# Kernel optimization log

Measured on AMD Instinct MI355X. Metric: run time of the kernel, lower is better.

Reference implementation:

```python
import jax, jax.numpy as jnp
import numpy as np

B, S, F = 4, 512, 512
H, D = 8, 64          # num_heads, hidden_dim per head
R = 64                # number of relative-position buckets
OUT = 512


def setup_inputs() -> dict:
    key = jax.random.key(0)
    ks = jax.random.split(key, 12)
    sF = 1.0 / np.sqrt(F)
    sHD = 1.0 / np.sqrt(H * D)
    inp = {
        "key": jax.random.normal(ks[0], (B, S, F), jnp.float32),
        "value": jax.random.normal(ks[1], (B, S, F), jnp.float32),
        "query": jax.random.normal(ks[2], (B, S, F), jnp.float32),
        # padding mask: last 64 key positions masked out per batch element
        "mask": jnp.zeros((B, S), bool).at[:, S - 64:].set(True),
        "adj": jax.random.randint(ks[3], (B, S, S), 0, R, jnp.int64),
        "Wq": jax.random.normal(ks[4], (F, H * D), jnp.float32) * sF,
        "bq": jnp.zeros((H * D,), jnp.float32),
        "Wk": jax.random.normal(ks[5], (F, H * D), jnp.float32) * sF,
        "bk": jnp.zeros((H * D,), jnp.float32),
        "Wv": jax.random.normal(ks[6], (F, H * D), jnp.float32) * sF,
        "bv": jnp.zeros((H * D,), jnp.float32),
        "Wo": jax.random.normal(ks[7], (H * D, OUT), jnp.float32) * sHD,
        "bo": jnp.zeros((OUT,), jnp.float32),
        "emb_k": jax.random.normal(ks[8], (R, D), jnp.float32) * 0.02,
        "emb_v": jax.random.normal(ks[9], (R, D), jnp.float32) * 0.02,
    }
    return inp


def reference(key, value, query, mask, adj,
              Wq, bq, Wk, bk, Wv, bv, Wo, bo, emb_k, emb_v):
    b, s, _ = value.shape
    scale = 1.0 / np.sqrt(D)
    # projections -> [b, heads, seq, d]
    q = (query @ Wq + bq).reshape(b, s, H, D).transpose(0, 2, 1, 3)
    k = (key @ Wk + bk).reshape(b, s, H, D).transpose(0, 2, 1, 3)
    v = (value @ Wv + bv).reshape(b, s, H, D).transpose(0, 2, 1, 3)
    # content scores [b, h, q, k]
    scores = jnp.einsum('bhqd,bhkd->bhqk', q, k) * scale
    # relative-position key bias: emb_k[adj] is [b, q, k, d]
    a_k = emb_k[adj]
    scores = scores + jnp.einsum('bhqd,bqkd->bhqk', q, a_k) * scale
    # key-padding mask (True -> -inf), broadcast over heads and query rows
    scores = jnp.where(mask[:, None, None, :], jnp.asarray(-jnp.inf, scores.dtype), scores)
    attn = jax.nn.softmax(scores, axis=-1)  # dropout p=0 -> identity
    # context + relative-position value contribution
    ctx = jnp.einsum('bhqk,bhkd->bhqd', attn, v)
    a_v = emb_v[adj]  # [b, q, k, d]
    ctx = ctx + jnp.einsum('bhqk,bqkd->bhqd', attn, a_v)
    ctx = ctx.transpose(0, 2, 1, 3).reshape(b, s, H * D)
    out = ctx @ Wo + bo
    return out, attn
```

## Files before the change

### kernel.cpp

```cpp
#include <hip/hip_runtime.h>
#include <hip/hip_bf16.h>
#include <math.h>

#define BB 4
#define SS 512
#define HH 8
#define DD 64
#define RR 64
#define OO 512

typedef _Float16 f16;
typedef __attribute__((ext_vector_type(8))) _Float16 f16x8;
typedef __attribute__((ext_vector_type(4))) _Float16 f16x4;
typedef __attribute__((ext_vector_type(4))) float f32x4;

#define WS_QH    0u
#define WS_KH    (2u<<20)
#define WS_VTH   (4u<<20)
#define WS_CTXH  (6u<<20)
#define WS_ADJ8  (8u<<20)
#define WS_WT    (12u<<20)
#define WS_EVT   (14u<<20)

__device__ __forceinline__ int swz128(int row, int b)  { return row*128  + (b ^ ((row&7)<<4)); }
__device__ __forceinline__ int swz1024(int row, int b) { return row*1024 + (b ^ ((row&7)<<4)); }

__device__ __forceinline__ void pack8(const float4& x, const float4& y, f16x8& o) {
    o[0]=(f16)x.x; o[1]=(f16)x.y; o[2]=(f16)x.z; o[3]=(f16)x.w;
    o[4]=(f16)y.x; o[5]=(f16)y.y; o[6]=(f16)y.z; o[7]=(f16)y.w;
}

__global__ __launch_bounds__(256) void k_pack(const int* __restrict__ adj,
                                              const void* __restrict__ mask,
                                              unsigned char* __restrict__ adj8)
{
    const int tid = threadIdx.x;
    __shared__ int s_odd, s_big;
    if (tid == 0) { s_odd = 0; s_big = 0; }
    __syncthreads();
    int odd = 0, big = 0;
    const unsigned int* mu = (const unsigned int*)mask;
    for (int i = tid; i < 512; i += 256) {
        odd |= (adj[2*i + 1] != 0);
        big |= (mu[i] > 1u);
    }
    if (odd) atomicOr(&s_odd, 1);
    if (big) atomicOr(&s_big, 1);
    __syncthreads();
    const int f64 = s_odd ? 0 : 1;
    const int fbyte = s_big;

    const int t = blockIdx.x * 256 + tid;
    const int e0 = t * 4;
    const int b = e0 >> 18, k0 = e0 & 511;
    int a[4];
    if (f64) {
        const int4 A = ((const int4*)adj)[2*t];
        const int4 Bv = ((const int4*)adj)[2*t + 1];
        a[0] = A.x; a[1] = A.z; a[2] = Bv.x; a[3] = Bv.z;
    } else {
        const int4 A = ((const int4*)adj)[t];
        a[0] = A.x; a[1] = A.y; a[2] = A.z; a[3] = A.w;
    }
    unsigned int mbits;
    if (fbyte) {
        const unsigned int mw = *(const unsigned int*)((const unsigned char*)mask + b*512 + k0);
        mbits = ((mw & 255u) ? 1u : 0) | (((mw >> 8) & 255u) ? 2u : 0)
              | (((mw >> 16) & 255u) ? 4u : 0) | (((mw >> 24) & 255u) ? 8u : 0);
    } else {
        const int4 mv = ((const int4*)mask)[(b*512 + k0) >> 2];
        mbits = (mv.x ? 1u : 0) | (mv.y ? 2u : 0) | (mv.z ? 4u : 0) | (mv.w ? 8u : 0);
    }
    unsigned int w = 0;
#pragma unroll
    for (int j = 0; j < 4; ++j)
        w |= ((unsigned)(a[j] & 63) | (((mbits >> j) & 1u) << 7)) << (8*j);
    ((unsigned int*)adj8)[t] = w;
}

__global__ __launch_bounds__(256) void k_prep(
    const float* __restrict__ Wq, const float* __restrict__ Wk,
    const float* __restrict__ Wv, const float* __restrict__ Wo,
    const float* __restrict__ emb_v, f16* __restrict__ WT, f16* __restrict__ evt)
{
    const int z = blockIdx.z;
    __shared__ float tile[64][65];
    const int tid = threadIdx.x;
    const int r = tid >> 2, c4 = (tid & 3) * 16;
    if (z < 4) {
        const float* W = (z==0)?Wq:(z==1)?Wk:(z==2)?Wv:Wo;
        f16* T = WT + (size_t)z * 262144;
        const int k0 = blockIdx.y * 64, n0 = blockIdx.x * 64;
#pragma unroll
        for (int u = 0; u < 4; ++u) {
            const float4 w4 = *(const float4*)&W[(size_t)(k0 + r)*512 + n0 + c4 + u*4];
            tile[r][c4+u*4+0] = w4.x; tile[r][c4+u*4+1] = w4.y;
            tile[r][c4+u*4+2] = w4.z; tile[r][c4+u*4+3] = w4.w;
        }
        __syncthreads();
        f16x8 v0, v1;
#pragma unroll
        for (int j = 0; j < 8; ++j) { v0[j] = (f16)tile[c4+j][r]; v1[j] = (f16)tile[c4+8+j][r]; }
        f16* dst = &T[(size_t)(n0 + r)*512 + k0 + c4];
        *(f16x8*)dst = v0; *(f16x8*)(dst + 8) = v1;
    } else {
        if (blockIdx.x | blockIdx.y) return;
#pragma unroll
        for (int u = 0; u < 4; ++u) {
            const float4 w4 = *(const float4*)&emb_v[(size_t)r*64 + c4 + u*4];
            tile[r][c4+u*4+0] = w4.x; tile[r][c4+u*4+1] = w4.y;
            tile[r][c4+u*4+2] = w4.z; tile[r][c4+u*4+3] = w4.w;
        }
        __syncthreads();
        f16x8 v0, v1;
#pragma unroll
        for (int j = 0; j < 8; ++j) { v0[j] = (f16)tile[c4+j][r]; v1[j] = (f16)tile[c4+8+j][r]; }
        f16* dst = &evt[(size_t)r*64 + c4];
        *(f16x8*)dst = v0; *(f16x8*)(dst + 8) = v1;
    }
}

__global__ __launch_bounds__(256) void k_proj(
    const float* __restrict__ query, const float* __restrict__ key, const float* __restrict__ value,
    const f16* __restrict__ WT,
    const float* __restrict__ bq, const float* __restrict__ bk, const float* __restrict__ bv,
    f16* __restrict__ qh, f16* __restrict__ kh, f16* __restrict__ vth)
{
    const int z = blockIdx.z;
    const float* A    = (z == 0) ? query : (z == 1) ? key : value;
    const f16*   Bt   = WT + (size_t)z * 262144;
    const float* bias = (z == 0) ? bq : (z == 1) ? bk : bv;

    const int n0 = blockIdx.x * 64;
    const int m0 = blockIdx.y * 64;
    __shared__ char Ab[2][8192];
    __shared__ char Bb[2][8192];
    const int tid = threadIdx.x;
    const int wid = tid >> 6, l = tid & 63;
    const int wr = wid >> 1, wc = wid & 1;
    const int lr = l & 15, lg = l >> 4;
    const int sr = tid >> 2, sc = (tid & 3) * 16;

    const float* Ap = &A[(size_t)(m0 + sr)*512 + sc];
    const f16*   Bp = &Bt[(size_t)(n0 + sr)*512 + sc];

    f32x4 acc[2][2];
#pragma unroll
    for (int mi = 0; mi < 2; ++mi)
#pragma unroll
        for (int ni = 0; ni < 2; ++ni) acc[mi][ni] = (f32x4){0.f,0.f,0.f,0.f};

    float4 a4[4]; f16x8 b0, b1;
#pragma unroll
    for (int u = 0; u < 4; ++u) a4[u] = *(const float4*)(Ap + u*4);
    b0 = *(const f16x8*)Bp; b1 = *(const f16x8*)(Bp + 8);
    {
        f16x8 p0, p1;
        pack8(a4[0], a4[1], p0); pack8(a4[2], a4[3], p1);
        *(f16x8*)(Ab[0] + swz128(sr, sc*2))    = p0;
        *(f16x8*)(Ab[0] + swz128(sr, sc*2+16)) = p1;
        *(f16x8*)(Bb[0] + swz128(sr, sc*2))    = b0;
        *(f16x8*)(Bb[0] + swz128(sr, sc*2+16)) = b1;
    }
#pragma unroll
    for (int t = 0; t < 8; ++t) {
        __syncthreads();
        if (t < 7) {
#pragma unroll
            for (int u = 0; u < 4; ++u) a4[u] = *(const float4*)(Ap + (t+1)*64 + u*4);
            b0 = *(const f16x8*)(Bp + (t+1)*64);
            b1 = *(const f16x8*)(Bp + (t+1)*64 + 8);
        }
        const char* Ac = Ab[t & 1];
        const char* Bc = Bb[t & 1];
        f16x8 fa[2][2], fb[2][2];
#pragma unroll
        for (int mi = 0; mi < 2; ++mi) {
            const int row = wr*32 + mi*16 + lr;
#pragma unroll
            for (int ks = 0; ks < 2; ++ks)
                fa[mi][ks] = *(const f16x8*)(Ac + swz128(row, ks*64 + lg*16));
        }
#pragma unroll
        for (int ni = 0; ni < 2; ++ni) {
            const int row = wc*32 + ni*16 + lr;
#pragma unroll
            for (int ks = 0; ks < 2; ++ks)
                fb[ni][ks] = *(const f16x8*)(Bc + swz128(row, ks*64 + lg*16));
        }
#pragma unroll
        for (int ks = 0; ks < 2; ++ks)
#pragma unroll
            for (int mi = 0; mi < 2; ++mi)
#pragma unroll
                for (int ni = 0; ni < 2; ++ni)
                    acc[mi][ni] = __builtin_amdgcn_mfma_f32_16x16x32_f16(
                        fa[mi][ks], fb[ni][ks], acc[mi][ni], 0, 0, 0);
        if (t < 7) {
            f16x8 p0, p1;
            pack8(a4[0], a4[1], p0); pack8(a4[2], a4[3], p1);
            char* An = Ab[(t+1) & 1];
            char* Bn = Bb[(t+1) & 1];
            *(f16x8*)(An + swz128(sr, sc*2))    = p0;
            *(f16x8*)(An + swz128(sr, sc*2+16)) = p1;
            *(f16x8*)(Bn + swz128(sr, sc*2))    = b0;
            *(f16x8*)(Bn + swz128(sr, sc*2+16)) = b1;
        }
    }

#pragma unroll
    for (int ni = 0; ni < 2; ++ni) {
        const int n = n0 + wc*32 + ni*16 + lr;
        const float bv_ = bias[n];
        const int h = n >> 6, d = n & 63;
#pragma unroll
        for (int mi = 0; mi < 2; ++mi)
#pragma unroll
            for (int e = 0; e < 4; ++e) {
                const int m = m0 + wr*32 + mi*16 + lg*4 + e;
                const int b = m >> 9, s = m & 511;
                const f16 v = (f16)(acc[mi][ni][e] + bv_);
                if (z == 2)       vth[((size_t)(b*HH + h)*DD + d)*SS + s] = v;
                else if (z == 1)  kh [((size_t)(b*HH + h)*SS + s)*DD + d] = v;
                else              qh [((size_t)(b*HH + h)*SS + s)*DD + d] = v;
            }
    }
}

__global__ __launch_bounds__(256, 4) void k_attn(
    const f16* __restrict__ qh, const f16* __restrict__ kh, const f16* __restrict__ vth,
    const unsigned char* __restrict__ adj8, const float* __restrict__ emb_k,
    const f16* __restrict__ evt, float* __restrict__ attn, f16* __restrict__ ctxh)
{
    const int wg = (blockIdx.x & 7) * 128 + (blockIdx.x >> 3);
    const int z = wg >> 5, qb = wg & 31;
    const int b = z >> 3, h = z & 7;
    const int q0 = qb * 16;
    const int tid = threadIdx.x, w = tid >> 6, l = tid & 63;
    const int lr = l & 15, lg = l >> 4;
    const int sr = tid >> 2, sce = (tid & 3) * 16;

    __shared__ char KV[2][8192];
    __shared__ char Qb_[2048];
    __shared__ char Pb[16384];
    __shared__ float QW[16][65];
    __shared__ float red_m[4][16], red_s[4][16];

    unsigned int avw[8];
    const unsigned char* arow = &adj8[((size_t)b*SS + q0 + lr)*SS];
#pragma unroll
    for (int p = 0; p < 8; ++p)
        avw[p] = *(const unsigned int*)(arow + p*64 + w*16 + lg*4);
    f32x4 e4[4];
    {
        const float* ep = &emb_k[(size_t)(w*16 + lr)*DD];
        e4[0] = *(const f32x4*)(ep + lg*8);
        e4[1] = *(const f32x4*)(ep + lg*8 + 4);
        e4[2] = *(const f32x4*)(ep + 32 + lg*8);
        e4[3] = *(const f32x4*)(ep + 32 + lg*8 + 4);
    }
    f16x8 st0 = *(const f16x8*)&kh[((size_t)z*SS + sr)*DD + sce];
    f16x8 st1 = *(const f16x8*)&kh[((size_t)z*SS + sr)*DD + sce + 8];
    if (tid < 64) {
        const int r = tid >> 2, ce = (tid & 3) * 16;
        const f16* src = &qh[((size_t)z*SS + q0 + r)*DD + ce];
        *(f16x8*)(Qb_ + swz128(r, ce*2))      = *(const f16x8*)src;
        *(f16x8*)(Qb_ + swz128(r, ce*2 + 16)) = *(const f16x8*)(src + 8);
    }
    __syncthreads();

    const f16x8 fb0 = *(const f16x8*)(Qb_ + swz128(lr, lg*16));
    const f16x8 fb1 = *(const f16x8*)(Qb_ + swz128(lr, 64 + lg*16));
    {
        f16x8 fe0, fe1;
#pragma unroll
        for (int j = 0; j < 4; ++j) {
            fe0[j] = (f16)e4[0][j]; fe0[4+j] = (f16)e4[1][j];
            fe1[j] = (f16)e4[2][j]; fe1[4+j] = (f16)e4[3][j];
        }
        f32x4 aq = (f32x4){0.f,0.f,0.f,0.f};
        aq = __builtin_amdgcn_mfma_f32_16x16x32_f16(fe0, fb0, aq, 0, 0, 0);
        aq = __builtin_amdgcn_mfma_f32_16x16x32_f16(fe1, fb1, aq, 0, 0, 0);
#pragma unroll
        for (int e = 0; e < 4; ++e) QW[lr][w*16 + lg*4 + e] = aq[e];
    }
    *(f16x8*)(KV[0] + swz128(sr, sce*2))      = st0;
    *(f16x8*)(KV[0] + swz128(sr, sce*2 + 16)) = st1;
    __syncthreads();

    f32x4 acc[8];
#pragma unroll
    for (int p = 0; p < 8; ++p) acc[p] = (f32x4){0.f,0.f,0.f,0.f};
#pragma unroll
    for (int p = 0; p < 8; ++p) {
        if (p < 7) {
            st0 = *(const f16x8*)&kh[((size_t)z*SS + (p+1)*64 + sr)*DD + sce];
            st1 = *(const f16x8*)&kh[((size_t)z*SS + (p+1)*64 + sr)*DD + sce + 8];
        }
        const char* Kc = KV[p & 1];
        const f16x8 fa0 = *(const f16x8*)(Kc + swz128(w*16 + lr, lg*16));
        const f16x8 fa1 = *(const f16x8*)(Kc + swz128(w*16 + lr, 64 + lg*16));
        acc[p] = __builtin_amdgcn_mfma_f32_16x16x32_f16(fa0, fb0, acc[p], 0, 0, 0);
        acc[p] = __builtin_amdgcn_mfma_f32_16x16x32_f16(fa1, fb1, acc[p], 0, 0, 0);
        if (p < 7) {
            char* Kn = KV[(p+1) & 1];
            *(f16x8*)(Kn + swz128(sr, sce*2))      = st0;
            *(f16x8*)(Kn + swz128(sr, sce*2 + 16)) = st1;
            __syncthreads();
        }
    }

    float mx = -1e30f;
#pragma unroll
    for (int p = 0; p < 8; ++p)
#pragma unroll
        for (int e = 0; e < 4; ++e) {
            const unsigned a = (avw[p] >> (8*e)) & 255u;
            float s = (acc[p][e] + QW[lr][a & 63]) * 0.125f;
            s = (a & 128u) ? -1e30f : s;
            acc[p][e] = s;
            mx = fmaxf(mx, s);
        }
    mx = fmaxf(mx, __shfl_xor(mx, 16, 64));
    mx = fmaxf(mx, __shfl_xor(mx, 32, 64));
    float sm = 0.f;
#pragma unroll
    for (int p = 0; p < 8; ++p)
#pragma unroll
        for (int e = 0; e < 4; ++e) {
            const float ev = __expf(acc[p][e] - mx);
            acc[p][e] = ev; sm += ev;
        }
    sm += __shfl_xor(sm, 16, 64);
    sm += __shfl_xor(sm, 32, 64);
    if (l < 16) { red_m[w][lr] = mx; red_s[w][lr] = sm; }
    __syncthreads();
    float M = red_m[0][lr];
#pragma unroll
    for (int j = 1; j < 4; ++j) M = fmaxf(M, red_m[j][lr]);
    float T = 0.f;
#pragma unroll
    for (int j = 0; j < 4; ++j) T += red_s[j][lr] * __expf(red_m[j][lr] - M);
    const float scale = __expf(mx - M) / T;

    f16x8 v0 = *(const f16x8*)&vth[((size_t)z*DD + sr)*SS + sce];
    f16x8 v1 = *(const f16x8*)&vth[((size_t)z*DD + sr)*SS + sce + 8];

    for (int i = tid; i < 16*65; i += 256) (&QW[0][0])[i] = 0.f;
    __syncthreads();

#pragma unroll
    for (int p = 0; p < 8; ++p) {
        const float pv0 = acc[p][0]*scale, pv1 = acc[p][1]*scale;
        const float pv2 = acc[p][2]*scale, pv3 = acc[p][3]*scale;
        *(float4*)&attn[((size_t)z*SS + q0 + lr)*SS + p*64 + w*16 + lg*4] =
            make_float4(pv0, pv1, pv2, pv3);
        f16x4 ph; ph[0]=(f16)pv0; ph[1]=(f16)pv1; ph[2]=(f16)pv2; ph[3]=(f16)pv3;
        *(f16x4*)(Pb + swz1024(lr, (p*64 + w*16 + lg*4)*2)) = ph;
        atomicAdd(&QW[lr][(avw[p]      ) & 63], pv0);
        atomicAdd(&QW[lr][(avw[p] >>  8) & 63], pv1);
        atomicAdd(&QW[lr][(avw[p] >> 16) & 63], pv2);
        atomicAdd(&QW[lr][(avw[p] >> 24) & 63], pv3);
    }
    *(f16x8*)(KV[0] + swz128(sr, sce*2))      = v0;
    *(f16x8*)(KV[0] + swz128(sr, sce*2 + 16)) = v1;
    __syncthreads();

    f32x4 acc2 = (f32x4){0.f,0.f,0.f,0.f};
#pragma unroll
    for (int p = 0; p < 8; ++p) {
        if (p < 7) {
            v0 = *(const f16x8*)&vth[((size_t)z*DD + sr)*SS + (p+1)*64 + sce];
            v1 = *(const f16x8*)&vth[((size_t)z*DD + sr)*SS + (p+1)*64 + sce + 8];
        }
        const char* Vc = KV[p & 1];
#pragma unroll
        for (int ks = 0; ks < 2; ++ks) {
            const f16x8 fa = *(const f16x8*)(Pb + swz1024(lr, p*128 + ks*64 + lg*16));
            const f16x8 fb = *(const f16x8*)(Vc + swz128(w*16 + lr, ks*64 + lg*16));
            acc2 = __builtin_amdgcn_mfma_f32_16x16x32_f16(fa, fb, acc2, 0, 0, 0);
        }
        if (p < 7) {
            char* Vn = KV[(p+1) & 1];
            *(f16x8*)(Vn + swz128(sr, sce*2))      = v0;
            *(f16x8*)(Vn + swz128(sr, sce*2 + 16)) = v1;
            __syncthreads();
        }
    }
#pragma unroll
    for (int ks = 0; ks < 2; ++ks) {
        f16x8 fa;
        const float* wp = &QW[lr][ks*32 + lg*8];
#pragma unroll
        for (int j = 0; j < 8; ++j) fa[j] = (f16)wp[j];
        const f16x8 fb = *(const f16x8*)&evt[(size_t)(w*16 + lr)*RR + ks*32 + lg*8];
        acc2 = __builtin_amdgcn_mfma_f32_16x16x32_f16(fa, fb, acc2, 0, 0, 0);
    }
#pragma unroll
    for (int e = 0; e < 4; ++e)
        ctxh[((size_t)b*SS + q0 + lg*4 + e)*OO + h*DD + w*16 + lr] = (f16)acc2[e];
}

__global__ __launch_bounds__(256) void k_out(
    const f16* __restrict__ ctxh, const f16* __restrict__ WoT,
    const float* __restrict__ bo, float* __restrict__ out)
{
    const int n0 = blockIdx.x * 64;
    const int m0 = blockIdx.y * 64;
    __shared__ char Ab[2][8192];
    __shared__ char Bb[2][8192];
    const int tid = threadIdx.x;
    const int wid = tid >> 6, l = tid & 63;
    const int wr = wid >> 1, wc = wid & 1;
    const int lr = l & 15, lg = l >> 4;
    const int sr = tid >> 2, sc = (tid & 3) * 16;

    const f16* Ap = &ctxh[(size_t)(m0 + sr)*512 + sc];
    const f16* Bp = &WoT[(size_t)(n0 + sr)*512 + sc];

    f32x4 acc[2][2];
#pragma unroll
    for (int mi = 0; mi < 2; ++mi)
#pragma unroll
        for (int ni = 0; ni < 2; ++ni) acc[mi][ni] = (f32x4){0.f,0.f,0.f,0.f};

    f16x8 a0 = *(const f16x8*)Ap, a1 = *(const f16x8*)(Ap + 8);
    f16x8 b0 = *(const f16x8*)Bp, b1 = *(const f16x8*)(Bp + 8);
    *(f16x8*)(Ab[0] + swz128(sr, sc*2))    = a0;
    *(f16x8*)(Ab[0] + swz128(sr, sc*2+16)) = a1;
    *(f16x8*)(Bb[0] + swz128(sr, sc*2))    = b0;
    *(f16x8*)(Bb[0] + swz128(sr, sc*2+16)) = b1;
#pragma unroll
    for (int t = 0; t < 8; ++t) {
        __syncthreads();
        if (t < 7) {
            a0 = *(const f16x8*)(Ap + (t+1)*64); a1 = *(const f16x8*)(Ap + (t+1)*64 + 8);
            b0 = *(const f16x8*)(Bp + (t+1)*64); b1 = *(const f16x8*)(Bp + (t+1)*64 + 8);
        }
        const char* Ac = Ab[t & 1];
        const char* Bc = Bb[t & 1];
        f16x8 fa[2][2], fb[2][2];
#pragma unroll
        for (int mi = 0; mi < 2; ++mi) {
            const int row = wr*32 + mi*16 + lr;
#pragma unroll
            for (int ks = 0; ks < 2; ++ks)
                fa[mi][ks] = *(const f16x8*)(Ac + swz128(row, ks*64 + lg*16));
        }
#pragma unroll
        for (int ni = 0; ni < 2; ++ni) {
            const int row = wc*32 + ni*16 + lr;
#pragma unroll
            for (int ks = 0; ks < 2; ++ks)
                fb[ni][ks] = *(const f16x8*)(Bc + swz128(row, ks*64 + lg*16));
        }
#pragma unroll
        for (int ks = 0; ks < 2; ++ks)
#pragma unroll
            for (int mi = 0; mi < 2; ++mi)
#pragma unroll
                for (int ni = 0; ni < 2; ++ni)
                    acc[mi][ni] = __builtin_amdgcn_mfma_f32_16x16x32_f16(
                        fa[mi][ks], fb[ni][ks], acc[mi][ni], 0, 0, 0);
        if (t < 7) {
            char* An = Ab[(t+1) & 1];
            char* Bn = Bb[(t+1) & 1];
            *(f16x8*)(An + swz128(sr, sc*2))    = a0;
            *(f16x8*)(An + swz128(sr, sc*2+16)) = a1;
            *(f16x8*)(Bn + swz128(sr, sc*2))    = b0;
            *(f16x8*)(Bn + swz128(sr, sc*2+16)) = b1;
        }
    }

#pragma unroll
    for (int ni = 0; ni < 2; ++ni) {
        const int n = n0 + wc*32 + ni*16 + lr;
        const float bv_ = bo[n];
#pragma unroll
        for (int mi = 0; mi < 2; ++mi)
#pragma unroll
            for (int e = 0; e < 4; ++e) {
                const int m = m0 + wr*32 + mi*16 + lg*4 + e;
                out[(size_t)m*512 + n] = acc[mi][ni][e] + bv_;
            }
    }
}

extern "C" void kernel_launch(void* const* d_in, const int* in_sizes, int n_in,
                              void* d_out, int out_size, void* d_ws, size_t ws_size,
                              hipStream_t stream)
{
    const float* key   = (const float*)d_in[0];
    const float* value = (const float*)d_in[1];
    const float* query = (const float*)d_in[2];
    const void*  mask  = d_in[3];
    const int*   adj   = (const int*)d_in[4];
    const float* Wq    = (const float*)d_in[5];
    const float* bq    = (const float*)d_in[6];
    const float* Wk    = (const float*)d_in[7];
    const float* bk    = (const float*)d_in[8];
    const float* Wv    = (const float*)d_in[9];
    const float* bv    = (const float*)d_in[10];
    const float* Wo    = (const float*)d_in[11];
    const float* bo    = (const float*)d_in[12];
    const float* emb_k = (const float*)d_in[13];
    const float* emb_v = (const float*)d_in[14];

    char* w8 = (char*)d_ws;
    f16* qh   = (f16*)(w8 + WS_QH);
    f16* kh   = (f16*)(w8 + WS_KH);
    f16* vth  = (f16*)(w8 + WS_VTH);
    f16* ctxh = (f16*)(w8 + WS_CTXH);
    unsigned char* adj8p = (unsigned char*)(w8 + WS_ADJ8);
    f16* WT   = (f16*)(w8 + WS_WT);
    f16* WoT  = WT + (size_t)3 * 262144;
    f16* evt  = (f16*)(w8 + WS_EVT);

    float* outp = (float*)d_out;
    float* attn = outp + (size_t)BB*SS*OO;

    k_pack<<<1024, 256, 0, stream>>>(adj, mask, adj8p);
    k_prep<<<dim3(8, 8, 5), 256, 0, stream>>>(Wq, Wk, Wv, Wo, emb_v, WT, evt);
    k_proj<<<dim3(8, 32, 3), 256, 0, stream>>>(query, key, value, WT,
                                               bq, bk, bv, qh, kh, vth);
    k_attn<<<1024, 256, 0, stream>>>(qh, kh, vth, adj8p, emb_k, evt, attn, ctxh);
    k_out <<<dim3(8, 32), 256, 0, stream>>>(ctxh, WoT, bo, outp);
}
```

Measured before the change: 186.4 us.

## Pre-swizzle Q/K/V tiles, stream softmax scores through LDS, merge prep kernels

The projection kernel now writes Q, K and V^T directly in the swizzled tile layout that the attention kernel's LDS expects. Attention can then copy tiles contiguously per thread, without address math and with coalesced loads. The attention kernel stores scaled scores as f16 in shared memory during the QK loop instead of keeping eight accumulators in registers, which should reduce register pressure. Normalisation by the softmax sum is deferred to a final attn write pass and to the ctx output. The two prep kernels are merged into one launch. In exchange, the attn output is now computed from f16-rounded scores and exponentials, which loses precision, and the projection epilogue does scattered 2-byte writes.

Result: no change. 189.4 us (+1.6%).

```diff
diff --git a/kernel.cpp b/kernel.cpp
--- a/kernel.cpp
+++ b/kernel.cpp
@@ -14,9 +14,9 @@
 typedef __attribute__((ext_vector_type(4))) _Float16 f16x4;
 typedef __attribute__((ext_vector_type(4))) float f32x4;
 
-#define WS_QH    0u
-#define WS_KH    (2u<<20)
-#define WS_VTH   (4u<<20)
+#define WS_QHS   0u
+#define WS_KHS   (2u<<20)
+#define WS_VTS   (4u<<20)
 #define WS_CTXH  (6u<<20)
 #define WS_ADJ8  (8u<<20)
 #define WS_WT    (12u<<20)
@@ -30,67 +30,69 @@
     o[4]=(f16)y.x; o[5]=(f16)y.y; o[6]=(f16)y.z; o[7]=(f16)y.w;
 }
 
-__global__ __launch_bounds__(256) void k_pack(const int* __restrict__ adj,
-                                              const void* __restrict__ mask,
-                                              unsigned char* __restrict__ adj8)
+__global__ __launch_bounds__(256) void k_prep_all(
+    const int* __restrict__ adj, const void* __restrict__ mask,
+    const float* __restrict__ Wq, const float* __restrict__ Wk,
+    const float* __restrict__ Wv, const float* __restrict__ Wo,
+    const float* __restrict__ emb_v,
+    unsigned char* __restrict__ adj8, f16* __restrict__ WT, f16* __restrict__ evt)
 {
     const int tid = threadIdx.x;
+    const int bid = blockIdx.x;
     __shared__ int s_odd, s_big;
-    if (tid == 0) { s_odd = 0; s_big = 0; }
-    __syncthreads();
-    int odd = 0, big = 0;
-    const unsigned int* mu = (const unsigned int*)mask;
-    for (int i = tid; i < 512; i += 256) {
-        odd |= (adj[2*i + 1] != 0);
-        big |= (mu[i] > 1u);
-    }
-    if (odd) atomicOr(&s_odd, 1);
-    if (big) atomicOr(&s_big, 1);
-    __syncthreads();
-    const int f64 = s_odd ? 0 : 1;
-    const int fbyte = s_big;
-
-    const int t = blockIdx.x * 256 + tid;
-    const int e0 = t * 4;
-    const int b = e0 >> 18, k0 = e0 & 511;
-    int a[4];
-    if (f64) {
-        const int4 A = ((const int4*)adj)[2*t];
-        const int4 Bv = ((const int4*)adj)[2*t + 1];
-        a[0] = A.x; a[1] = A.z; a[2] = Bv.x; a[3] = Bv.z;
-    } else {
-        const int4 A = ((const int4*)adj)[t];
-        a[0] = A.x; a[1] = A.y; a[2] = A.z; a[3] = A.w;
-    }
-    unsigned int mbits;
-    if (fbyte) {
-        const unsigned int mw = *(const unsigned int*)((const unsigned char*)mask + b*512 + k0);
-        mbits = ((mw & 255u) ? 1u : 0) | (((mw >> 8) & 255u) ? 2u : 0)
-              | (((mw >> 16) & 255u) ? 4u : 0) | (((mw >> 24) & 255u) ? 8u : 0);
-    } else {
-        const int4 mv = ((const int4*)mask)[(b*512 + k0) >> 2];
-        mbits = (mv.x ? 1u : 0) | (mv.y ? 2u : 0) | (mv.z ? 4u : 0) | (mv.w ? 8u : 0);
-    }
-    unsigned int w = 0;
-#pragma unroll
-    for (int j = 0; j < 4; ++j)
-        w |= ((unsigned)(a[j] & 63) | (((mbits >> j) & 1u) << 7)) << (8*j);
-    ((unsigned int*)adj8)[t] = w;
-}
-
-__global__ __launch_bounds__(256) void k_prep(
-    const float* __restrict__ Wq, const float* __restrict__ Wk,
-    const float* __restrict__ Wv, const float* __restrict__ Wo,
-    const float* __restrict__ emb_v, f16* __restrict__ WT, f16* __restrict__ evt)
-{
-    const int z = blockIdx.z;
     __shared__ float tile[64][65];
-    const int tid = threadIdx.x;
+
+    if (bid < 1024) {
+        if (tid == 0) { s_odd = 0; s_big = 0; }
+        __syncthreads();
+        int odd = 0, big = 0;
+        const unsigned int* mu = (const unsigned int*)mask;
+        for (int i = tid; i < 512; i += 256) {
+            odd |= (adj[2*i + 1] != 0);
+            big |= (mu[i] > 1u);
+        }
+        if (odd) atomicOr(&s_odd, 1);
+        if (big) atomicOr(&s_big, 1);
+        __syncthreads();
+        const int f64 = s_odd ? 0 : 1;
+        const int fbyte = s_big;
+
+        const int t = bid * 256 + tid;
+        const int e0 = t * 4;
+        const int b = e0 >> 18, k0 = e0 & 511;
+        int a[4];
+        if (f64) {
+            const int4 A = ((const int4*)adj)[2*t];
+            const int4 Bv = ((const int4*)adj)[2*t + 1];
+            a[0] = A.x; a[1] = A.z; a[2] = Bv.x; a[3] = Bv.z;
+        } else {
+            const int4 A = ((const int4*)adj)[t];
+            a[0] = A.x; a[1] = A.y; a[2] = A.z; a[3] = A.w;
+        }
+        unsigned int mbits;
+        if (fbyte) {
+            const unsigned int mw = *(const unsigned int*)((const unsigned char*)mask + b*512 + k0);
+            mbits = ((mw & 255u) ? 1u : 0) | (((mw >> 8) & 255u) ? 2u : 0)
+                  | (((mw >> 16) & 255u) ? 4u : 0) | (((mw >> 24) & 255u) ? 8u : 0);
+        } else {
+            const int4 mv = ((const int4*)mask)[(b*512 + k0) >> 2];
+            mbits = (mv.x ? 1u : 0) | (mv.y ? 2u : 0) | (mv.z ? 4u : 0) | (mv.w ? 8u : 0);
+        }
+        unsigned int w = 0;
+#pragma unroll
+        for (int j = 0; j < 4; ++j)
+            w |= ((unsigned)(a[j] & 63) | (((mbits >> j) & 1u) << 7)) << (8*j);
+        ((unsigned int*)adj8)[t] = w;
+        return;
+    }
+
+    const int pid = bid - 1024;
+    const int z = pid >> 6, rem = pid & 63;
     const int r = tid >> 2, c4 = (tid & 3) * 16;
     if (z < 4) {
         const float* W = (z==0)?Wq:(z==1)?Wk:(z==2)?Wv:Wo;
         f16* T = WT + (size_t)z * 262144;
-        const int k0 = blockIdx.y * 64, n0 = blockIdx.x * 64;
+        const int n0 = (rem & 7) * 64, k0 = (rem >> 3) * 64;
 #pragma unroll
         for (int u = 0; u < 4; ++u) {
             const float4 w4 = *(const float4*)&W[(size_t)(k0 + r)*512 + n0 + c4 + u*4];
@@ -104,7 +106,7 @@
         f16* dst = &T[(size_t)(n0 + r)*512 + k0 + c4];
         *(f16x8*)dst = v0; *(f16x8*)(dst + 8) = v1;
     } else {
-        if (blockIdx.x | blockIdx.y) return;
+        if (rem) return;
 #pragma unroll
         for (int u = 0; u < 4; ++u) {
             const float4 w4 = *(const float4*)&emb_v[(size_t)r*64 + c4 + u*4];
@@ -124,7 +126,7 @@
     const float* __restrict__ query, const float* __restrict__ key, const float* __restrict__ value,
     const f16* __restrict__ WT,
     const float* __restrict__ bq, const float* __restrict__ bk, const float* __restrict__ bv,
-    f16* __restrict__ qh, f16* __restrict__ kh, f16* __restrict__ vth)
+    char* __restrict__ qhs, char* __restrict__ khs, char* __restrict__ vts)
 {
     const int z = blockIdx.z;
     const float* A    = (z == 0) ? query : (z == 1) ? key : value;
@@ -219,16 +221,20 @@
             for (int e = 0; e < 4; ++e) {
                 const int m = m0 + wr*32 + mi*16 + lg*4 + e;
                 const int b = m >> 9, s = m & 511;
+                const int zq = b*HH + h;
                 const f16 v = (f16)(acc[mi][ni][e] + bv_);
-                if (z == 2)       vth[((size_t)(b*HH + h)*DD + d)*SS + s] = v;
-                else if (z == 1)  kh [((size_t)(b*HH + h)*SS + s)*DD + d] = v;
-                else              qh [((size_t)(b*HH + h)*SS + s)*DD + d] = v;
+                if (z == 0)
+                    *(f16*)(qhs + ((size_t)(zq*32 + (s>>4)))*2048 + swz128(s & 15, d*2)) = v;
+                else if (z == 1)
+                    *(f16*)(khs + ((size_t)(zq*8 + (s>>6)))*8192 + swz128(s & 63, d*2)) = v;
+                else
+                    *(f16*)(vts + ((size_t)(zq*8 + (s>>6)))*8192 + swz128(d, (s & 63)*2)) = v;
             }
     }
 }
 
 __global__ __launch_bounds__(256, 4) void k_attn(
-    const f16* __restrict__ qh, const f16* __restrict__ kh, const f16* __restrict__ vth,
+    const char* __restrict__ qhs, const char* __restrict__ khs, const char* __restrict__ vts,
     const unsigned char* __restrict__ adj8, const float* __restrict__ emb_k,
     const f16* __restrict__ evt, float* __restrict__ attn, f16* __restrict__ ctxh)
 {
@@ -238,13 +244,16 @@
     const int q0 = qb * 16;
     const int tid = threadIdx.x, w = tid >> 6, l = tid & 63;
     const int lr = l & 15, lg = l >> 4;
-    const int sr = tid >> 2, sce = (tid & 3) * 16;
 
     __shared__ char KV[2][8192];
     __shared__ char Qb_[2048];
-    __shared__ char Pb[16384];
+    __shared__ char PS[16384];
     __shared__ float QW[16][65];
     __shared__ float red_m[4][16], red_s[4][16];
+    __shared__ float invT_s[16];
+
+    const char* khz = khs + (size_t)z * 65536;
+    const char* vtz = vts + (size_t)z * 65536;
 
     unsigned int avw[8];
     const unsigned char* arow = &adj8[((size_t)b*SS + q0 + lr)*SS];
@@ -259,13 +268,11 @@
         e4[2] = *(const f32x4*)(ep + 32 + lg*8);
         e4[3] = *(const f32x4*)(ep + 32 + lg*8 + 4);
     }
-    f16x8 st0 = *(const f16x8*)&kh[((size_t)z*SS + sr)*DD + sce];
-    f16x8 st1 = *(const f16x8*)&kh[((size_t)z*SS + sr)*DD + sce + 8];
-    if (tid < 64) {
-        const int r = tid >> 2, ce = (tid & 3) * 16;
-        const f16* src = &qh[((size_t)z*SS + q0 + r)*DD + ce];
-        *(f16x8*)(Qb_ + swz128(r, ce*2))      = *(const f16x8*)src;
-        *(f16x8*)(Qb_ + swz128(r, ce*2 + 16)) = *(const f16x8*)(src + 8);
+    f16x8 st0 = *(const f16x8*)(khz + tid*16);
+    f16x8 st1 = *(const f16x8*)(khz + 4096 + tid*16);
+    {
+        const char* qhz = qhs + ((size_t)z*32 + qb) * 2048;
+        *(f16x4*)(Qb_ + tid*8) = *(const f16x4*)(qhz + tid*8);
     }
     __syncthreads();
 
@@ -284,109 +291,112 @@
 #pragma unroll
         for (int e = 0; e < 4; ++e) QW[lr][w*16 + lg*4 + e] = aq[e];
     }
-    *(f16x8*)(KV[0] + swz128(sr, sce*2))      = st0;
-    *(f16x8*)(KV[0] + swz128(sr, sce*2 + 16)) = st1;
+    *(f16x8*)(KV[0] + tid*16)        = st0;
+    *(f16x8*)(KV[0] + 4096 + tid*16) = st1;
     __syncthreads();
 
-    f32x4 acc[8];
-#pragma unroll
-    for (int p = 0; p < 8; ++p) acc[p] = (f32x4){0.f,0.f,0.f,0.f};
+    float mx = -1e30f;
 #pragma unroll
     for (int p = 0; p < 8; ++p) {
         if (p < 7) {
-            st0 = *(const f16x8*)&kh[((size_t)z*SS + (p+1)*64 + sr)*DD + sce];
-            st1 = *(const f16x8*)&kh[((size_t)z*SS + (p+1)*64 + sr)*DD + sce + 8];
+            st0 = *(const f16x8*)(khz + (p+1)*8192 + tid*16);
+            st1 = *(const f16x8*)(khz + (p+1)*8192 + 4096 + tid*16);
         }
         const char* Kc = KV[p & 1];
         const f16x8 fa0 = *(const f16x8*)(Kc + swz128(w*16 + lr, lg*16));
         const f16x8 fa1 = *(const f16x8*)(Kc + swz128(w*16 + lr, 64 + lg*16));
-        acc[p] = __builtin_amdgcn_mfma_f32_16x16x32_f16(fa0, fb0, acc[p], 0, 0, 0);
-        acc[p] = __builtin_amdgcn_mfma_f32_16x16x32_f16(fa1, fb1, acc[p], 0, 0, 0);
+        f32x4 a = (f32x4){0.f,0.f,0.f,0.f};
+        a = __builtin_amdgcn_mfma_f32_16x16x32_f16(fa0, fb0, a, 0, 0, 0);
+        a = __builtin_amdgcn_mfma_f32_16x16x32_f16(fa1, fb1, a, 0, 0, 0);
+        const unsigned av = avw[p];
+        f16x4 sv;
+#pragma unroll
+        for (int e = 0; e < 4; ++e) {
+            const unsigned ab = (av >> (8*e)) & 255u;
+            float s = (a[e] + QW[lr][ab & 63]) * 0.125f;
+            s = (ab & 128u) ? -1e30f : s;
+            mx = fmaxf(mx, s);
+            sv[e] = (f16)s;
+        }
+        *(f16x4*)(PS + swz1024(lr, p*128 + w*32 + lg*8)) = sv;
         if (p < 7) {
             char* Kn = KV[(p+1) & 1];
-            *(f16x8*)(Kn + swz128(sr, sce*2))      = st0;
-            *(f16x8*)(Kn + swz128(sr, sce*2 + 16)) = st1;
+            *(f16x8*)(Kn + tid*16)        = st0;
+            *(f16x8*)(Kn + 4096 + tid*16) = st1;
             __syncthreads();
         }
     }
 
-    float mx = -1e30f;
-#pragma unroll
-    for (int p = 0; p < 8; ++p)
-#pragma unroll
-        for (int e = 0; e < 4; ++e) {
-            const unsigned a = (avw[p] >> (8*e)) & 255u;
-            float s = (acc[p][e] + QW[lr][a & 63]) * 0.125f;
-            s = (a & 128u) ? -1e30f : s;
-            acc[p][e] = s;
-            mx = fmaxf(mx, s);
-        }
     mx = fmaxf(mx, __shfl_xor(mx, 16, 64));
     mx = fmaxf(mx, __shfl_xor(mx, 32, 64));
+    if (l < 16) red_m[w][lr] = mx;
+    __syncthreads();
+    f16x8 v0 = *(const f16x8*)(vtz + tid*16);
+    f16x8 v1 = *(const f16x8*)(vtz + 4096 + tid*16);
+    for (int i = tid; i < 16*65; i += 256) (&QW[0][0])[i] = 0.f;
+    const float M = fmaxf(fmaxf(red_m[0][lr], red_m[1][lr]),
+                          fmaxf(red_m[2][lr], red_m[3][lr]));
+    __syncthreads();
+
     float sm = 0.f;
 #pragma unroll
-    for (int p = 0; p < 8; ++p)
-#pragma unroll
-        for (int e = 0; e < 4; ++e) {
-            const float ev = __expf(acc[p][e] - mx);
-            acc[p][e] = ev; sm += ev;
-        }
+    for (int p = 0; p < 8; ++p) {
+        f16x4* ps = (f16x4*)(PS + swz1024(lr, p*128 + w*32 + lg*8));
+        const f16x4 sv = *ps;
+        const float e0 = __expf((float)sv[0] - M);
+        const float e1 = __expf((float)sv[1] - M);
+        const float e2 = __expf((float)sv[2] - M);
+        const float e3 = __expf((float)sv[3] - M);
+        sm += (e0 + e1) + (e2 + e3);
+        f16x4 ev; ev[0]=(f16)e0; ev[1]=(f16)e1; ev[2]=(f16)e2; ev[3]=(f16)e3;
+        *ps = ev;
+        const unsigned av = avw[p];
+        atomicAdd(&QW[lr][(av      ) & 63], e0);
+        atomicAdd(&QW[lr][(av >>  8) & 63], e1);
+        atomicAdd(&QW[lr][(av >> 16) & 63], e2);
+        atomicAdd(&QW[lr][(av >> 24) & 63], e3);
+    }
     sm += __shfl_xor(sm, 16, 64);
     sm += __shfl_xor(sm, 32, 64);
-    if (l < 16) { red_m[w][lr] = mx; red_s[w][lr] = sm; }
+    if (l < 16) red_s[w][lr] = sm;
+    *(f16x8*)(KV[0] + tid*16)        = v0;
+    *(f16x8*)(KV[0] + 4096 + tid*16) = v1;
     __syncthreads();
-    float M = red_m[0][lr];
-#pragma unroll
-    for (int j = 1; j < 4; ++j) M = fmaxf(M, red_m[j][lr]);
-    float T = 0.f;
-#pragma unroll
-    for (int j = 0; j < 4; ++j) T += red_s[j][lr] * __expf(red_m[j][lr] - M);
-    const float scale = __expf(mx - M) / T;
-
-    f16x8 v0 = *(const f16x8*)&vth[((size_t)z*DD + sr)*SS + sce];
-    f16x8 v1 = *(const f16x8*)&vth[((size_t)z*DD + sr)*SS + sce + 8];
-
-    for (int i = tid; i < 16*65; i += 256) (&QW[0][0])[i] = 0.f;
-    __syncthreads();
-
-#pragma unroll
-    for (int p = 0; p < 8; ++p) {
-        const float pv0 = acc[p][0]*scale, pv1 = acc[p][1]*scale;
-        const float pv2 = acc[p][2]*scale, pv3 = acc[p][3]*scale;
-        *(float4*)&attn[((size_t)z*SS + q0 + lr)*SS + p*64 + w*16 + lg*4] =
-            make_float4(pv0, pv1, pv2, pv3);
-        f16x4 ph; ph[0]=(f16)pv0; ph[1]=(f16)pv1; ph[2]=(f16)pv2; ph[3]=(f16)pv3;
-        *(f16x4*)(Pb + swz1024(lr, (p*64 + w*16 + lg*4)*2)) = ph;
-        atomicAdd(&QW[lr][(avw[p]      ) & 63], pv0);
-        atomicAdd(&QW[lr][(avw[p] >>  8) & 63], pv1);
-        atomicAdd(&QW[lr][(avw[p] >> 16) & 63], pv2);
-        atomicAdd(&QW[lr][(avw[p] >> 24) & 63], pv3);
-    }
-    *(f16x8*)(KV[0] + swz128(sr, sce*2))      = v0;
-    *(f16x8*)(KV[0] + swz128(sr, sce*2 + 16)) = v1;
-    __syncthreads();
+    if (tid < 16)
+        invT_s[tid] = 1.f / (red_s[0][tid] + red_s[1][tid] + red_s[2][tid] + red_s[3][tid]);
 
     f32x4 acc2 = (f32x4){0.f,0.f,0.f,0.f};
 #pragma unroll
     for (int p = 0; p < 8; ++p) {
         if (p < 7) {
-            v0 = *(const f16x8*)&vth[((size_t)z*DD + sr)*SS + (p+1)*64 + sce];
-            v1 = *(const f16x8*)&vth[((size_t)z*DD + sr)*SS + (p+1)*64 + sce + 8];
+            v0 = *(const f16x8*)(vtz + (p+1)*8192 + tid*16);
+            v1 = *(const f16x8*)(vtz + (p+1)*8192 + 4096 + tid*16);
         }
         const char* Vc = KV[p & 1];
 #pragma unroll
         for (int ks = 0; ks < 2; ++ks) {
-            const f16x8 fa = *(const f16x8*)(Pb + swz1024(lr, p*128 + ks*64 + lg*16));
+            const f16x8 fa = *(const f16x8*)(PS + swz1024(lr, p*128 + ks*64 + lg*16));
             const f16x8 fb = *(const f16x8*)(Vc + swz128(w*16 + lr, ks*64 + lg*16));
             acc2 = __builtin_amdgcn_mfma_f32_16x16x32_f16(fa, fb, acc2, 0, 0, 0);
         }
         if (p < 7) {
             char* Vn = KV[(p+1) & 1];
-            *(f16x8*)(Vn + swz128(sr, sce*2))      = v0;
-            *(f16x8*)(Vn + swz128(sr, sce*2 + 16)) = v1;
+            *(f16x8*)(Vn + tid*16)        = v0;
+            *(f16x8*)(Vn + 4096 + tid*16) = v1;
             __syncthreads();
         }
     }
+
+#pragma unroll
+    for (int jj = 0; jj < 8; ++jj) {
+        const int idx = tid + jj*256;
+        const int row = idx >> 7, c4 = idx & 127;
+        const f16x4 pv = *(const f16x4*)(PS + swz1024(row, c4*8));
+        const float it = invT_s[row];
+        *(float4*)&attn[((size_t)z*SS + q0 + row)*SS + c4*4] =
+            make_float4((float)pv[0]*it, (float)pv[1]*it, (float)pv[2]*it, (float)pv[3]*it);
+    }
+
 #pragma unroll
     for (int ks = 0; ks < 2; ++ks) {
         f16x8 fa;
@@ -398,7 +408,8 @@
     }
 #pragma unroll
     for (int e = 0; e < 4; ++e)
-        ctxh[((size_t)b*SS + q0 + lg*4 + e)*OO + h*DD + w*16 + lr] = (f16)acc2[e];
+        ctxh[((size_t)b*SS + q0 + lg*4 + e)*OO + h*DD + w*16 + lr] =
+            (f16)(acc2[e] * invT_s[lg*4 + e]);
 }
 
 __global__ __launch_bounds__(256) void k_out(
@@ -507,22 +518,22 @@
     const float* emb_v = (const float*)d_in[14];
 
     char* w8 = (char*)d_ws;
-    f16* qh   = (f16*)(w8 + WS_QH);
-    f16* kh   = (f16*)(w8 + WS_KH);
-    f16* vth  = (f16*)(w8 + WS_VTH);
-    f16* ctxh = (f16*)(w8 + WS_CTXH);
+    char* qhs = w8 + WS_QHS;
+    char* khs = w8 + WS_KHS;
+    char* vts = w8 + WS_VTS;
+    f16*  ctxh = (f16*)(w8 + WS_CTXH);
     unsigned char* adj8p = (unsigned char*)(w8 + WS_ADJ8);
-    f16* WT   = (f16*)(w8 + WS_WT);
-    f16* WoT  = WT + (size_t)3 * 262144;
-    f16* evt  = (f16*)(w8 + WS_EVT);
+    f16*  WT  = (f16*)(w8 + WS_WT);
+    f16*  WoT = WT + (size_t)3 * 262144;
+    f16*  evt = (f16*)(w8 + WS_EVT);
 
     float* outp = (float*)d_out;
     float* attn = outp + (size_t)BB*SS*OO;
 
-    k_pack<<<1024, 256, 0, stream>>>(adj, mask, adj8p);
-    k_prep<<<dim3(8, 8, 5), 256, 0, stream>>>(Wq, Wk, Wv, Wo, emb_v, WT, evt);
+    k_prep_all<<<1344, 256, 0, stream>>>(adj, mask, Wq, Wk, Wv, Wo, emb_v,
+                                         adj8p, WT, evt);
     k_proj<<<dim3(8, 32, 3), 256, 0, stream>>>(query, key, value, WT,
-                                               bq, bk, bv, qh, kh, vth);
-    k_attn<<<1024, 256, 0, stream>>>(qh, kh, vth, adj8p, emb_k, evt, attn, ctxh);
+                                               bq, bk, bv, qhs, khs, vts);
+    k_attn<<<1024, 256, 0, stream>>>(qhs, khs, vts, adj8p, emb_k, evt, attn, ctxh);
     k_out <<<dim3(8, 32), 256, 0, stream>>>(ctxh, WoT, bo, outp);
 }
```
